# Optimization experiments

Measured on AMD Instinct MI355X. Metric: run time of the kernel, lower is better.

The kernel has to match this reference:

```python
import jax, jax.numpy as jnp
import numpy as np

S = 1.0 / np.sqrt(2.0).astype(np.float32)  # Haar normalization


def _dwt_axis(x, axis):
    """Level-1 Haar DWT along `axis` (length must be even).
    Returns (lo, hi), each half-length along axis."""
    x = jnp.moveaxis(x, axis, -1)
    n = x.shape[-1]
    xp = x.reshape(x.shape[:-1] + (n // 2, 2))
    lo = (xp[..., 0] + xp[..., 1]) * S
    hi = (xp[..., 0] - xp[..., 1]) * S
    return jnp.moveaxis(lo, -1, axis), jnp.moveaxis(hi, -1, axis)


def _idwt_axis(lo, hi, axis, orig_len):
    """Inverse level-1 Haar along `axis`: interleave (lo+hi)*s, (lo-hi)*s."""
    lo = jnp.moveaxis(lo, axis, -1)
    hi = jnp.moveaxis(hi, axis, -1)
    even = (lo + hi) * S
    odd = (lo - hi) * S
    rec = jnp.stack([even, odd], axis=-1).reshape(lo.shape[:-1] + (2 * lo.shape[-1],))
    rec = rec[..., :orig_len]
    return jnp.moveaxis(rec, -1, axis)


def _mix(sub, W, b):
    # 1x1 conv = channel mixing: (B,C,H,W), W: (Cout,Cin), b: (Cout,)
    return jnp.einsum('oc,bchw->bohw', W, sub) + b[None, :, None, None]


def setup_inputs() -> dict:
    key = jax.random.key(0)
    B, C, H, W = 8, 64, 256, 256
    ks = jax.random.split(key, 9)
    scale = 1.0 / C
    inp = {'x': jax.random.normal(ks[0], (B, C, H, W), dtype=jnp.float32)}
    for i, name in enumerate(['LL', 'LH', 'HL', 'HH']):
        inp[f'w_{name}'] = jax.random.uniform(ks[1 + i], (C, C), jnp.float32, -scale, scale)
        inp[f'b_{name}'] = jnp.zeros((C,), jnp.float32)
    return inp


def reference(x, w_LL, b_LL, w_LH, b_LH, w_HL, b_HL, w_HH, b_HH):
    B, C, H, W = x.shape
    # DWT: along W then along H (separable Haar)
    Lw, Hw = _dwt_axis(x, -1)
    LL, LH = _dwt_axis(Lw, -2)
    HL, HH = _dwt_axis(Hw, -2)
    # Per-subband 1x1 channel mixers
    LL = _mix(LL, w_LL, b_LL)
    LH = _mix(LH, w_LH, b_LH)
    HL = _mix(HL, w_HL, b_HL)
    HH = _mix(HH, w_HH, b_HH)
    # IDWT: along H then along W
    Lw_r = _idwt_axis(LL, LH, -2, H)
    Hw_r = _idwt_axis(HL, HH, -2, H)
    return _idwt_axis(Lw_r, Hw_r, -1, W)
```

## Files before the change

kernel.cpp:

```cpp
#include <hip/hip_runtime.h>
#include <hip/hip_bf16.h>


using bf16x8 = __attribute__((ext_vector_type(8))) short;
using f32x4  = __attribute__((ext_vector_type(4))) float;

__device__ inline unsigned short f2bf(float v) {
    __hip_bfloat16 h = __float2bfloat16(v);
    return __builtin_bit_cast(unsigned short, h);
}

__global__ __launch_bounds__(256) void wvc_prep(
    const float* __restrict__ wLL, const float* __restrict__ bLL,
    const float* __restrict__ wLH, const float* __restrict__ bLH,
    const float* __restrict__ wHL, const float* __restrict__ bHL,
    const float* __restrict__ wHH, const float* __restrict__ bHH,
    unsigned short* __restrict__ afrag, float* __restrict__ bcomb)
{
    const int idx  = blockIdx.x * 256 + threadIdx.x;
    const int i    = idx & 7;
    const int lane = (idx >> 3) & 63;
    const int mt   = (idx >> 9) & 3;
    const int ks   = (idx >> 11) & 1;
    const int band = (idx >> 12) & 3;
    const float* Ws[4] = {wLL, wLH, wHL, wHH};
    const int o = mt * 16 + (lane & 15);
    const int c = ks * 32 + (lane >> 4) * 8 + i;
    afrag[idx] = f2bf(0.5f * Ws[band][o * 64 + c]);

    if (blockIdx.x == 0 && threadIdx.x < 64) {
        const int t = threadIdx.x;
        float b0 = bLL[t], b1 = bLH[t], b2 = bHL[t], b3 = bHH[t];
        bcomb[0 * 64 + t] = 0.5f * (b0 + b1 + b2 + b3);
        bcomb[1 * 64 + t] = 0.5f * (b0 + b1 - b2 - b3);
        bcomb[2 * 64 + t] = 0.5f * (b0 - b1 + b2 - b3);
        bcomb[3 * 64 + t] = 0.5f * (b0 - b1 - b2 + b3);
    }
}

#define NT 8
__global__ __launch_bounds__(256, 2) void wvc_main(
    const float* __restrict__ x,
    const unsigned short* __restrict__ afrag_g,
    const float* __restrict__ bcomb,
    float* __restrict__ out)
{
    __shared__ __align__(64) unsigned char lds_x[2][33024];
    __shared__ __align__(16) float lds_bc[256];

    const int tid = threadIdx.x;
    const int l   = tid & 63;
    const int wv  = tid >> 6;
    const int blk = blockIdx.x;
    const int b   = blk >> 6;
    const int jq  = (blk >> 4) & 3;
    const int ig  = blk & 15;
    const int w0  = jq * 64;

    const int sg   = wv & 1;
    const int m0   = (wv >> 1) * 2;
    const int site = sg * 16 + (l & 15);
    const int lg   = l >> 4;

    lds_bc[tid] = bcomb[tid];

    const unsigned short* afb = afrag_g + (size_t)l * 8;
    bf16x8 a[4][2][2];
    #pragma unroll
    for (int bd = 0; bd < 4; ++bd)
        #pragma unroll
        for (int ks = 0; ks < 2; ++ks)
            #pragma unroll
            for (int mtl = 0; mtl < 2; ++mtl)
                a[bd][ks][mtl] = *(const bf16x8*)(
                    afb + (size_t)((bd * 2 + ks) * 4 + m0 + mtl) * 512);

    const float* xb = x + (size_t)b * 4194304
                        + (size_t)(wv * 16 + (l >> 5)) * 65536
                        + (size_t)((l >> 4) & 1) * 256 + w0 + (l & 15) * 4;
    const int lbo = (wv * 16) * 512 + (wv * 2) * 32;

    {
        const float* g = xb + (size_t)(ig * 8 + 0) * 512;
        unsigned char* lbn = &lds_x[0][lbo];
        #pragma unroll
        for (int k = 0; k < 8; ++k)
            __builtin_amdgcn_global_load_lds(
                (const __attribute__((address_space(1))) void*)(g + (size_t)(2 * k) * 65536),
                (__attribute__((address_space(3))) void*)(lbn + k * 1024 + (k >> 2) * 32),
                16, 0, 0);
    }
    asm volatile("s_waitcnt lgkmcnt(0)" ::: "memory");

    for (int t = 0; t < NT; ++t) {
        if (t + 1 < NT) {
            const float* g = xb + (size_t)(ig * 8 + t + 1) * 512;
            unsigned char* lbn = &lds_x[(t + 1) & 1][lbo];
            #pragma unroll
            for (int k = 0; k < 8; ++k)
                __builtin_amdgcn_global_load_lds(
                    (const __attribute__((address_space(1))) void*)(g + (size_t)(2 * k) * 65536),
                    (__attribute__((address_space(3))) void*)(lbn + k * 1024 + (k >> 2) * 32),
                    16, 0, 0);
        }
        if (t == 0)            asm volatile("s_waitcnt vmcnt(8)"  ::: "memory");
        else if (t + 1 < NT)   asm volatile("s_waitcnt vmcnt(24)" ::: "memory");
        else                   asm volatile("s_waitcnt vmcnt(16)" ::: "memory");
        __builtin_amdgcn_sched_barrier(0);
        __builtin_amdgcn_s_barrier();
        __builtin_amdgcn_sched_barrier(0);

        const unsigned char* bx = lds_x[t & 1];

        bf16x8 bfr[4][2];
        #pragma unroll
        for (int ks = 0; ks < 2; ++ks) {
            float2 p0[8], p1[8];
            #pragma unroll
            for (int i = 0; i < 8; ++i) {
                const unsigned char* base =
                    bx + (size_t)(ks * 32 + lg * 8 + i) * 512
                       + (ks * 4 + lg) * 32 + site * 8;
                p0[i] = *(const float2*)(base);
                p1[i] = *(const float2*)(base + 256);
            }
            #pragma unroll
            for (int i = 0; i < 8; ++i) {
                float aa = p0[i].x + p0[i].y, mm = p0[i].x - p0[i].y;
                float cc = p1[i].x + p1[i].y, dd = p1[i].x - p1[i].y;
                bfr[0][ks][i] = (short)f2bf(aa + cc);
                bfr[1][ks][i] = (short)f2bf(aa - cc);
                bfr[2][ks][i] = (short)f2bf(mm + dd);
                bfr[3][ks][i] = (short)f2bf(mm - dd);
            }
        }

        f32x4 acc[4][2];
        #pragma unroll
        for (int bd = 0; bd < 4; ++bd)
            #pragma unroll
            for (int mtl = 0; mtl < 2; ++mtl)
                acc[bd][mtl] = (f32x4){0.f, 0.f, 0.f, 0.f};
        #pragma unroll
        for (int bd = 0; bd < 4; ++bd)
            #pragma unroll
            for (int ks = 0; ks < 2; ++ks)
                #pragma unroll
                for (int mtl = 0; mtl < 2; ++mtl)
                    acc[bd][mtl] = __builtin_amdgcn_mfma_f32_16x16x32_bf16(
                        a[bd][ks][mtl], bfr[bd][ks], acc[bd][mtl], 0, 0, 0);

        const int h0 = (ig * 8 + t) * 2;
        float* ob = out + (size_t)b * 4194304 + (size_t)h0 * 256 + w0 + 2 * site;
        #pragma unroll
        for (int mtl = 0; mtl < 2; ++mtl) {
            const int ob0 = (m0 + mtl) * 16 + lg * 4;
            f32x4 bc0 = *(const f32x4*)(&lds_bc[  0 + ob0]);
            f32x4 bc1 = *(const f32x4*)(&lds_bc[ 64 + ob0]);
            f32x4 bc2 = *(const f32x4*)(&lds_bc[128 + ob0]);
            f32x4 bc3 = *(const f32x4*)(&lds_bc[192 + ob0]);
            #pragma unroll
            for (int r = 0; r < 4; ++r) {
                float y0 = acc[0][mtl][r];
                float y1 = acc[1][mtl][r];
                float y2 = acc[2][mtl][r];
                float y3 = acc[3][mtl][r];
                float s01 = y0 + y1, d01 = y0 - y1;
                float s23 = y2 + y3, d23 = y2 - y3;
                float e00 = 0.5f * (s01 + s23) + bc0[r];
                float e01 = 0.5f * (s01 - s23) + bc1[r];
                float e10 = 0.5f * (d01 + d23) + bc2[r];
                float e11 = 0.5f * (d01 - d23) + bc3[r];
                float* po = ob + (size_t)(ob0 + r) * 65536;
                float2 v0; v0.x = e00; v0.y = e01;
                float2 v1; v1.x = e10; v1.y = e11;
                *(float2*)po         = v0;
                *(float2*)(po + 256) = v1;
            }
        }

        __builtin_amdgcn_sched_barrier(0);
        __builtin_amdgcn_s_barrier();
        __builtin_amdgcn_sched_barrier(0);
    }
}

extern "C" void kernel_launch(void* const* d_in, const int* in_sizes, int n_in,
                              void* d_out, int out_size, void* d_ws, size_t ws_size,
                              hipStream_t stream) {
    const float* x   = (const float*)d_in[0];
    const float* wLL = (const float*)d_in[1];
    const float* bLL = (const float*)d_in[2];
    const float* wLH = (const float*)d_in[3];
    const float* bLH = (const float*)d_in[4];
    const float* wHL = (const float*)d_in[5];
    const float* bHL = (const float*)d_in[6];
    const float* wHH = (const float*)d_in[7];
    const float* bHH = (const float*)d_in[8];
    float* out = (float*)d_out;

    unsigned short* afrag = (unsigned short*)d_ws;
    float* bcomb = (float*)((char*)d_ws + 32768);

    wvc_prep<<<64, 256, 0, stream>>>(wLL, bLL, wLH, bLH, wHL, bHL, wHH, bHH,
                                     afrag, bcomb);
    wvc_main<<<512, 256, 0, stream>>>(x, afrag, bcomb, out);
}
```

Baseline: 54.83 us.

## Use 512-thread blocks with triple-buffered LDS prefetch and nontemporal stores

Doubles the block size to 8 waves, so each wave owns one output-channel tile instead of two, and halves the grid while each block processes 16 row pairs. Input staging goes from double to triple buffering with a prefetch distance of two tiles, and the vmcnt waits are retuned to match. Output writes become nontemporal stores. The aim is to hide more global-load latency and reduce cache pollution from the write stream. The cost is fewer blocks per CU (launch bounds 512,1), larger LDS use and a smaller grid of 256 blocks.

```diff
diff --git a/kernel.cpp b/kernel.cpp
--- a/kernel.cpp
+++ b/kernel.cpp
@@ -4,6 +4,7 @@
 
 using bf16x8 = __attribute__((ext_vector_type(8))) short;
 using f32x4  = __attribute__((ext_vector_type(4))) float;
+using f32x2  = __attribute__((ext_vector_type(2))) float;
 
 __device__ inline unsigned short f2bf(float v) {
     __hip_bfloat16 h = __float2bfloat16(v);
@@ -38,79 +39,80 @@
     }
 }
 
-#define NT 8
-__global__ __launch_bounds__(256, 2) void wvc_main(
+#define NT 16
+__global__ __launch_bounds__(512, 1) void wvc_main(
     const float* __restrict__ x,
     const unsigned short* __restrict__ afrag_g,
     const float* __restrict__ bcomb,
     float* __restrict__ out)
 {
-    __shared__ __align__(64) unsigned char lds_x[2][33024];
+    __shared__ __align__(64) unsigned char lds_x[3][33024];
     __shared__ __align__(16) float lds_bc[256];
 
     const int tid = threadIdx.x;
     const int l   = tid & 63;
     const int wv  = tid >> 6;
     const int blk = blockIdx.x;
-    const int b   = blk >> 6;
-    const int jq  = (blk >> 4) & 3;
-    const int ig  = blk & 15;
+    const int b   = blk >> 5;
+    const int jq  = (blk >> 3) & 3;
+    const int ih  = blk & 7;
     const int w0  = jq * 64;
 
     const int sg   = wv & 1;
-    const int m0   = (wv >> 1) * 2;
+    const int mt   = wv >> 1;
     const int site = sg * 16 + (l & 15);
     const int lg   = l >> 4;
 
-    lds_bc[tid] = bcomb[tid];
+    if (tid < 256) lds_bc[tid] = bcomb[tid];
 
     const unsigned short* afb = afrag_g + (size_t)l * 8;
-    bf16x8 a[4][2][2];
+    bf16x8 a[4][2];
     #pragma unroll
     for (int bd = 0; bd < 4; ++bd)
         #pragma unroll
         for (int ks = 0; ks < 2; ++ks)
-            #pragma unroll
-            for (int mtl = 0; mtl < 2; ++mtl)
-                a[bd][ks][mtl] = *(const bf16x8*)(
-                    afb + (size_t)((bd * 2 + ks) * 4 + m0 + mtl) * 512);
+            a[bd][ks] = *(const bf16x8*)(
+                afb + (size_t)((bd * 2 + ks) * 4 + mt) * 512);
 
     const float* xb = x + (size_t)b * 4194304
-                        + (size_t)(wv * 16 + (l >> 5)) * 65536
+                        + (size_t)(wv * 8 + (l >> 5)) * 65536
                         + (size_t)((l >> 4) & 1) * 256 + w0 + (l & 15) * 4;
-    const int lbo = (wv * 16) * 512 + (wv * 2) * 32;
-
-    {
-        const float* g = xb + (size_t)(ig * 8 + 0) * 512;
-        unsigned char* lbn = &lds_x[0][lbo];
-        #pragma unroll
-        for (int k = 0; k < 8; ++k)
+    const int lbo = wv * 4096 + wv * 32;
+
+    #pragma unroll
+    for (int pt = 0; pt < 2; ++pt) {
+        const float* g = xb + (size_t)(ih * 16 + pt) * 512;
+        unsigned char* lbn = &lds_x[pt][lbo];
+        #pragma unroll
+        for (int k = 0; k < 4; ++k)
             __builtin_amdgcn_global_load_lds(
                 (const __attribute__((address_space(1))) void*)(g + (size_t)(2 * k) * 65536),
-                (__attribute__((address_space(3))) void*)(lbn + k * 1024 + (k >> 2) * 32),
+                (__attribute__((address_space(3))) void*)(lbn + k * 1024),
                 16, 0, 0);
     }
     asm volatile("s_waitcnt lgkmcnt(0)" ::: "memory");
 
+    #pragma unroll
     for (int t = 0; t < NT; ++t) {
-        if (t + 1 < NT) {
-            const float* g = xb + (size_t)(ig * 8 + t + 1) * 512;
-            unsigned char* lbn = &lds_x[(t + 1) & 1][lbo];
-            #pragma unroll
-            for (int k = 0; k < 8; ++k)
+        if (t + 2 < NT) {
+            const float* g = xb + (size_t)(ih * 16 + t + 2) * 512;
+            unsigned char* lbn = &lds_x[(t + 2) % 3][lbo];
+            #pragma unroll
+            for (int k = 0; k < 4; ++k)
                 __builtin_amdgcn_global_load_lds(
                     (const __attribute__((address_space(1))) void*)(g + (size_t)(2 * k) * 65536),
-                    (__attribute__((address_space(3))) void*)(lbn + k * 1024 + (k >> 2) * 32),
+                    (__attribute__((address_space(3))) void*)(lbn + k * 1024),
                     16, 0, 0);
         }
         if (t == 0)            asm volatile("s_waitcnt vmcnt(8)"  ::: "memory");
-        else if (t + 1 < NT)   asm volatile("s_waitcnt vmcnt(24)" ::: "memory");
-        else                   asm volatile("s_waitcnt vmcnt(16)" ::: "memory");
+        else if (t + 2 < NT)   asm volatile("s_waitcnt vmcnt(16)" ::: "memory");
+        else if (t + 1 < NT)   asm volatile("s_waitcnt vmcnt(12)" ::: "memory");
+        else                   asm volatile("s_waitcnt vmcnt(8)"  ::: "memory");
         __builtin_amdgcn_sched_barrier(0);
         __builtin_amdgcn_s_barrier();
         __builtin_amdgcn_sched_barrier(0);
 
-        const unsigned char* bx = lds_x[t & 1];
+        const unsigned char* bx = lds_x[t % 3];
 
         bf16x8 bfr[4][2];
         #pragma unroll
@@ -135,48 +137,39 @@
             }
         }
 
-        f32x4 acc[4][2];
+        f32x4 acc[4];
         #pragma unroll
         for (int bd = 0; bd < 4; ++bd)
-            #pragma unroll
-            for (int mtl = 0; mtl < 2; ++mtl)
-                acc[bd][mtl] = (f32x4){0.f, 0.f, 0.f, 0.f};
+            acc[bd] = (f32x4){0.f, 0.f, 0.f, 0.f};
         #pragma unroll
         for (int bd = 0; bd < 4; ++bd)
             #pragma unroll
             for (int ks = 0; ks < 2; ++ks)
-                #pragma unroll
-                for (int mtl = 0; mtl < 2; ++mtl)
-                    acc[bd][mtl] = __builtin_amdgcn_mfma_f32_16x16x32_bf16(
-                        a[bd][ks][mtl], bfr[bd][ks], acc[bd][mtl], 0, 0, 0);
-
-        const int h0 = (ig * 8 + t) * 2;
+                acc[bd] = __builtin_amdgcn_mfma_f32_16x16x32_bf16(
+                    a[bd][ks], bfr[bd][ks], acc[bd], 0, 0, 0);
+
+        const int h0 = (ih * 16 + t) * 2;
         float* ob = out + (size_t)b * 4194304 + (size_t)h0 * 256 + w0 + 2 * site;
-        #pragma unroll
-        for (int mtl = 0; mtl < 2; ++mtl) {
-            const int ob0 = (m0 + mtl) * 16 + lg * 4;
-            f32x4 bc0 = *(const f32x4*)(&lds_bc[  0 + ob0]);
-            f32x4 bc1 = *(const f32x4*)(&lds_bc[ 64 + ob0]);
-            f32x4 bc2 = *(const f32x4*)(&lds_bc[128 + ob0]);
-            f32x4 bc3 = *(const f32x4*)(&lds_bc[192 + ob0]);
-            #pragma unroll
-            for (int r = 0; r < 4; ++r) {
-                float y0 = acc[0][mtl][r];
-                float y1 = acc[1][mtl][r];
-                float y2 = acc[2][mtl][r];
-                float y3 = acc[3][mtl][r];
-                float s01 = y0 + y1, d01 = y0 - y1;
-                float s23 = y2 + y3, d23 = y2 - y3;
-                float e00 = 0.5f * (s01 + s23) + bc0[r];
-                float e01 = 0.5f * (s01 - s23) + bc1[r];
-                float e10 = 0.5f * (d01 + d23) + bc2[r];
-                float e11 = 0.5f * (d01 - d23) + bc3[r];
-                float* po = ob + (size_t)(ob0 + r) * 65536;
-                float2 v0; v0.x = e00; v0.y = e01;
-                float2 v1; v1.x = e10; v1.y = e11;
-                *(float2*)po         = v0;
-                *(float2*)(po + 256) = v1;
-            }
+        const int ob0 = mt * 16 + lg * 4;
+        f32x4 bc0 = *(const f32x4*)(&lds_bc[  0 + ob0]);
+        f32x4 bc1 = *(const f32x4*)(&lds_bc[ 64 + ob0]);
+        f32x4 bc2 = *(const f32x4*)(&lds_bc[128 + ob0]);
+        f32x4 bc3 = *(const f32x4*)(&lds_bc[192 + ob0]);
+        #pragma unroll
+        for (int r = 0; r < 4; ++r) {
+            float y0 = acc[0][r];
+            float y1 = acc[1][r];
+            float y2 = acc[2][r];
+            float y3 = acc[3][r];
+            float s01 = y0 + y1, d01 = y0 - y1;
+            float s23 = y2 + y3, d23 = y2 - y3;
+            f32x2 v0; v0[0] = 0.5f * (s01 + s23) + bc0[r];
+                      v0[1] = 0.5f * (s01 - s23) + bc1[r];
+            f32x2 v1; v1[0] = 0.5f * (d01 + d23) + bc2[r];
+                      v1[1] = 0.5f * (d01 - d23) + bc3[r];
+            float* po = ob + (size_t)(ob0 + r) * 65536;
+            __builtin_nontemporal_store(v0, (f32x2*)po);
+            __builtin_nontemporal_store(v1, (f32x2*)(po + 256));
         }
 
         __builtin_amdgcn_sched_barrier(0);
@@ -204,5 +197,5 @@
 
     wvc_prep<<<64, 256, 0, stream>>>(wLL, bLL, wLH, bLH, wHL, bHL, wHH, bHH,
                                      afrag, bcomb);
-    wvc_main<<<512, 256, 0, stream>>>(x, afrag, bcomb, out);
-}
+    wvc_main<<<256, 512, 0, stream>>>(x, afrag, bcomb, out);
+}
```

Result: faster. 52.66 us (-4.0%).
